# Kernel tuning notes

Hardware: AMD Instinct MI355X
Metric: run time of the kernel (lower is better)

The kernel has to match this reference:

```python
import jax, jax.numpy as jnp
import numpy as np

B, C, H, W = 4, 256, 64, 64
SCALE, K, COMP, G = 2, 5, 4, 1
MID = max(C // COMP, 16)                 # 64
ENC_OUT = K * K * SCALE * SCALE * G      # 100


def setup_inputs() -> dict:
    key = jax.random.key(0)
    k1, k2, k3 = jax.random.split(key, 3)
    x = jax.random.normal(k1, (B, C, H, W), jnp.float32)
    # comp: 1x1 conv C -> MID (store as matrix), enc: 3x3 conv MID -> ENC_OUT
    W_comp = jax.random.normal(k2, (MID, C), jnp.float32) * (1.0 / np.sqrt(C))
    b_comp = jnp.zeros((MID,), jnp.float32)
    W_enc = jax.random.normal(k3, (ENC_OUT, MID, 3, 3), jnp.float32) * (1.0 / np.sqrt(MID * 9))
    b_enc = jnp.zeros((ENC_OUT,), jnp.float32)
    return {"x": x, "W_comp": W_comp, "b_comp": b_comp, "W_enc": W_enc, "b_enc": b_enc}


def _unfold(x, k):
    """torch F.unfold with padding=(k-1)//2 -> (b, c, k*k, h, w), kh-major then kw."""
    b, c, h, w = x.shape
    p = (k - 1) // 2
    xp = jnp.pad(x, ((0, 0), (0, 0), (p, p), (p, p)))
    patches = jnp.stack(
        [xp[:, :, i:i + h, j:j + w] for i in range(k) for j in range(k)], axis=2
    )
    return patches  # (b, c, k*k, h, w)


def _carafe(x, W_comp, b_comp, W_enc, b_enc):
    b, c, h, w = x.shape
    s, k, g = SCALE, K, G
    # 1x1 compress conv + inplace relu
    feat = jax.nn.relu(jnp.einsum('bchw,mc->bmhw', x, W_comp) + b_comp[None, :, None, None])
    # 3x3 kernel-encoder conv, padding=1 (SAME)
    wk = jax.lax.conv_general_dilated(
        feat, W_enc, window_strides=(1, 1), padding='SAME',
        dimension_numbers=('NCHW', 'OIHW', 'NCHW')
    ) + b_enc[None, :, None, None]
    wk = wk.reshape(b, g, s * s, k * k, h, w)
    wk = jax.nn.softmax(wk, axis=3)  # softmax over k*k taps
    # unfold input and do the content-aware weighted gather-sum without the
    # (b,g,c/g,s*s,k*k,h,w) blow-up: contract over the k*k tap axis directly.
    xu = _unfold(x, k).reshape(b, g, c // g, k * k, h, w)
    out = jnp.einsum('bgpkhw,bgckhw->bgcphw', wk, xu)  # (b,g,c/g,s*s,h,w)
    # pixel rearrangement exactly as in the torch code:
    # view(b,c,s*s,h,w) -> permute(0,1,3,4,2) -> view(b,c,h*s,w*s)
    out = out.reshape(b, c, s * s, h, w)
    out = jnp.transpose(out, (0, 1, 3, 4, 2))
    out = out.reshape(b, c, h * s, w * s)
    return out


def reference(x, W_comp, b_comp, W_enc, b_enc):
    return _carafe(x, W_comp, b_comp, W_enc, b_enc)
```

## Files before the change

kernel.cpp:

```cpp
#include <hip/hip_runtime.h>

#define OFF_FEAT 0
#define OFF_WET  1048576
#define OFF_WCT  1122304
#define OFF_WK   1138688
#define WS_FLOATS 2777088

__global__ __launch_bounds__(256) void prep_kernel(
    const float* __restrict__ Wc, const float* __restrict__ We,
    float* __restrict__ ws) {
    int i = blockIdx.x * 256 + threadIdx.x;
    if (i < 16384) {
        int c = i >> 6, m = i & 63;
        ws[OFF_WCT + i] = Wc[m * 256 + c];
    }
    if (i < 73728) {
        int mrs = i >> 7, rem = i & 127;
        int p = rem >> 5, kk = rem & 31;
        ws[OFF_WET + i] = (kk < 25) ? We[(p * 25 + kk) * 576 + mrs] : 0.f;
    }
}

__global__ __launch_bounds__(256) void compress_kernel(
    const float* __restrict__ x, const float* __restrict__ bc,
    const float* __restrict__ ws, float* __restrict__ feat) {
    int blk = blockIdx.x;
    int pxg = blk >> 1, mh = blk & 1;
    int pixbase = pxg << 8;
    int b = pixbase >> 12, pl = pixbase & 4095;
    int t = threadIdx.x;
    const float* wct = ws + OFF_WCT + mh * 32;
    const float* xp = x + (((long long)b * 256) << 12) + pl + t;
    float acc[32];
#pragma unroll
    for (int q = 0; q < 32; q++) acc[q] = 0.f;
#pragma unroll 4
    for (int c = 0; c < 256; c++) {
        float xv = xp[(size_t)c << 12];
        const float* wr = wct + (c << 6);
#pragma unroll
        for (int q = 0; q < 32; q++) acc[q] += xv * wr[q];
    }
    int m0 = mh << 5;
#pragma unroll
    for (int q = 0; q < 32; q++) {
        float v = acc[q] + bc[m0 + q];
        feat[((b * 64 + m0 + q) << 12) + pl + t] = v > 0.f ? v : 0.f;
    }
}

__global__ __launch_bounds__(512, 4) void enc_kernel(
    const float* __restrict__ be, const float* __restrict__ ws,
    float* __restrict__ wkout) {
    __shared__ float fs[4224];
    int t = threadIdx.x;
    int blk = blockIdx.x;
    int tile = blk >> 1, ph2 = blk & 1;
    int b = tile >> 6, t6 = tile & 63;
    int i0 = (t6 >> 3) << 3, j0 = (t6 & 7) << 3;
    int pix = t & 63;
    int li = pix >> 3, lj = pix & 7;
    int g = __builtin_amdgcn_readfirstlane(t >> 6);
    int pp = g >> 2;
    int p = (ph2 << 1) | pp;
    int k0 = (g & 3) << 3;
    const float* feat = ws + OFF_FEAT;
    const float* wet = ws + OFF_WET + p * 32 + k0;

    float acc[8];
#pragma unroll
    for (int q = 0; q < 8; q++) acc[q] = 0.f;

    for (int phase = 0; phase < 2; phase++) {
        int mb = phase << 5;
        for (int idx = t; idx < 3200; idx += 512) {
            int m = idx / 100, pos = idx - m * 100;
            int r = pos / 10, s = pos - r * 10;
            int gi = i0 + r - 1, gj = j0 + s - 1;
            float v = 0.f;
            if ((unsigned)gi < 64u && (unsigned)gj < 64u)
                v = feat[(b * 64 + mb + m) * 4096 + (gi << 6) + gj];
            fs[m * 120 + r * 12 + s] = v;
        }
        __syncthreads();

#pragma unroll 2
        for (int m = 0; m < 32; m++) {
            const float* fb = fs + m * 120 + li * 12 + lj;
            float f9[9];
#pragma unroll
            for (int r = 0; r < 3; r++)
#pragma unroll
                for (int s = 0; s < 3; s++) f9[r * 3 + s] = fb[r * 12 + s];
            const float* wrow = wet + (mb + m) * 1152;
#pragma unroll
            for (int rs = 0; rs < 9; rs++) {
                float f = f9[rs];
                const float* wr = wrow + rs * 128;
#pragma unroll
                for (int q = 0; q < 8; q++) acc[q] += f * wr[q];
            }
        }
        __syncthreads();
    }

#pragma unroll
    for (int q = 0; q < 8; q++) {
        int k = k0 + q;
        if (k < 25) fs[pix * 66 + pp * 33 + k] = acc[q] + be[p * 25 + k];
    }
    __syncthreads();

    if (t < 128) {
        int sp = t >> 6, spx = t & 63;
        const float* lg = fs + spx * 66 + sp * 33;
        float sv[25], mx = -1e30f;
#pragma unroll
        for (int k = 0; k < 25; k++) { sv[k] = lg[k]; mx = fmaxf(mx, sv[k]); }
        float s = 0.f;
#pragma unroll
        for (int k = 0; k < 25; k++) { sv[k] = __expf(sv[k] - mx); s += sv[k]; }
        float inv = 1.f / s;
        int preal = (ph2 << 1) | sp;
        int pgl = ((i0 + (spx >> 3)) << 6) + j0 + (spx & 7);
        float* wp = wkout + (preal * 25) * 16384 + (b << 12) + pgl;
#pragma unroll
        for (int k = 0; k < 25; k++) wp[k * 16384] = sv[k] * inv;
    }
}

__global__ __launch_bounds__(256) void gather_kernel(
    const float* __restrict__ x, const float* __restrict__ ws,
    float* __restrict__ out) {
    __shared__ float xs[16 * 5 * 68];
    int t = threadIdx.x;
    int blk = blockIdx.x;
    int cc = blk & 15;
    int bi = blk >> 4;
    int b = bi >> 6, i = bi & 63;
    int j = t & 63;
    int g = t >> 6;
    int ph = g >> 1, ch = g & 1;

    float w0[25], w1[25];
    {
        const float* wp = ws + OFF_WK + (ph * 50) * 16384 + (b << 12) + (i << 6) + j;
#pragma unroll
        for (int k = 0; k < 25; k++) {
            w0[k] = wp[k * 16384];
            w1[k] = wp[(25 + k) * 16384];
        }
    }

    {
        int lane = t & 63, cd0 = t >> 6;
        for (int cd = cd0; cd < 80; cd += 4) {
            int c = cd / 5, dy = cd - c * 5;
            int gi = i - 2 + dy;
            float v = 0.f;
            if ((unsigned)gi < 64u)
                v = x[((b * 256 + (cc << 4) + c) << 12) + (gi << 6) + lane];
            float* row = xs + cd * 68;
            row[2 + lane] = v;
            if (lane < 2) row[lane] = 0.f;
            if (lane >= 62) row[lane + 4] = 0.f;
        }
    }
    __syncthreads();

    for (int c2 = ch; c2 < 16; c2 += 2) {
        const float* xb = xs + (c2 * 5) * 68 + j;
        float a0 = 0.f, a1 = 0.f;
#pragma unroll
        for (int dy = 0; dy < 5; dy++) {
#pragma unroll
            for (int dx = 0; dx < 5; dx++) {
                float xv = xb[dy * 68 + dx];
                int k = dy * 5 + dx;
                a0 += xv * w0[k];
                a1 += xv * w1[k];
            }
        }
        int c = (cc << 4) + c2;
        float2 o2 = make_float2(a0, a1);
        *(float2*)(out + (((b * 256 + c) << 12) + (i << 6) + j) * 4 + ph * 2) = o2;
    }
}

__global__ __launch_bounds__(512) void carafe_fused(
    const float* __restrict__ x, const float* __restrict__ Wc,
    const float* __restrict__ bc, const float* __restrict__ We,
    const float* __restrict__ be, float* __restrict__ out) {
    __shared__ float xs[32 * 144];
    __shared__ float fw[6656];
    __shared__ float wst[3600];
    const int t = threadIdx.x;
    const int blk = blockIdx.x;
    const int b = blk >> 6, tile = blk & 63;
    const int i0 = (tile >> 3) << 3, j0 = (tile & 7) << 3;
    const int wid = t >> 6, pix = t & 63;
    const int li = pix >> 3, lj = pix & 7;
    float facc[13];
#pragma unroll
    for (int q = 0; q < 13; q++) facc[q] = 0.f;
    for (int cc = 0; cc < 8; cc++) {
        for (int idx = t; idx < 32 * 144; idx += 512) {
            int c = idx / 144, pos = idx - c * 144;
            int r = pos / 12, u = pos - r * 12;
            int gi = i0 + r - 2, gj = j0 + u - 2;
            float v = 0.f;
            if ((unsigned)gi < 64u && (unsigned)gj < 64u)
                v = x[(((b * 256 + cc * 32 + c) << 12) + (gi << 6) + gj)];
            xs[idx] = v;
        }
        __syncthreads();
#pragma unroll
        for (int q = 0; q < 13; q++) {
            int idx = q * 512 + t;
            if (idx < 6400) {
                int m = idx / 100, pos = idx - m * 100;
                int fi = pos / 10, fj = pos - fi * 10;
                int tp = (fi + 1) * 12 + fj + 1;
                const float* wr = Wc + m * 256 + cc * 32;
                float a = facc[q];
                for (int c = 0; c < 32; c++) a += xs[c * 144 + tp] * wr[c];
                facc[q] = a;
            }
        }
        __syncthreads();
    }
#pragma unroll
    for (int q = 0; q < 13; q++) {
        int idx = q * 512 + t;
        if (idx < 6400) {
            int m = idx / 100, pos = idx - m * 100;
            int fi = pos / 10, fj = pos - fi * 10;
            int gi = i0 + fi - 1, gj = j0 + fj - 1;
            float v = facc[q] + bc[m];
            v = v > 0.f ? v : 0.f;
            if ((unsigned)gi >= 64u || (unsigned)gj >= 64u) v = 0.f;
            fw[idx] = v;
        }
    }
    float acc[13];
#pragma unroll
    for (int q = 0; q < 13; q++) acc[q] = 0.f;
    for (int mb = 0; mb < 16; mb++) {
        for (int idx = t; idx < 3600; idx += 512) {
            int mm = idx / 900, rem = idx - mm * 900;
            int o = rem / 9, rs = rem - o * 9;
            wst[idx] = We[o * 576 + (mb * 4 + mm) * 9 + rs];
        }
        __syncthreads();
#pragma unroll
        for (int mm = 0; mm < 4; mm++) {
            const float* fb = fw + (mb * 4 + mm) * 100 + li * 10 + lj;
            float f9[9];
#pragma unroll
            for (int r = 0; r < 3; r++)
#pragma unroll
                for (int s = 0; s < 3; s++) f9[r * 3 + s] = fb[r * 10 + s];
#pragma unroll
            for (int q = 0; q < 13; q++) {
                int o = q * 8 + wid;
                if (o < 100) {
                    const float* wr = wst + mm * 900 + o * 9;
                    float a = acc[q];
#pragma unroll
                    for (int rs = 0; rs < 9; rs++) a += f9[rs] * wr[rs];
                    acc[q] = a;
                }
            }
        }
        __syncthreads();
    }
#pragma unroll
    for (int q = 0; q < 13; q++) {
        int o = q * 8 + wid;
        if (o < 100) fw[pix * 104 + o] = acc[q];
    }
    __syncthreads();
    float sv[25];
    float inv = 0.f;
    const int sp = t >> 6, spx = t & 63;
    const bool act = (t < 256);
    if (act) {
        float mx = -1e30f;
#pragma unroll
        for (int k = 0; k < 25; k++) {
            sv[k] = fw[spx * 104 + sp * 25 + k] + be[sp * 25 + k];
            mx = fmaxf(mx, sv[k]);
        }
        float s = 0.f;
#pragma unroll
        for (int k = 0; k < 25; k++) { sv[k] = __expf(sv[k] - mx); s += sv[k]; }
        inv = 1.f / s;
    }
    __syncthreads();
    if (act) {
#pragma unroll
        for (int k = 0; k < 25; k++) fw[spx * 104 + k * 4 + sp] = sv[k] * inv;
    }
    __syncthreads();
    float w[25][4];
    const float4* wp = (const float4*)(fw + pix * 104);
#pragma unroll
    for (int k = 0; k < 25; k++) {
        float4 ww = wp[k];
        w[k][0] = ww.x; w[k][1] = ww.y; w[k][2] = ww.z; w[k][3] = ww.w;
    }
    const int pgl = ((i0 + li) << 6) + (j0 + lj);
    for (int cc = 0; cc < 8; cc++) {
        for (int idx = t; idx < 32 * 144; idx += 512) {
            int c = idx / 144, pos = idx - c * 144;
            int r = pos / 12, u = pos - r * 12;
            int gi = i0 + r - 2, gj = j0 + u - 2;
            float v = 0.f;
            if ((unsigned)gi < 64u && (unsigned)gj < 64u)
                v = x[(((b * 256 + cc * 32 + c) << 12) + (gi << 6) + gj)];
            xs[idx] = v;
        }
        __syncthreads();
        for (int c8 = wid; c8 < 32; c8 += 8) {
            const float* xc = xs + c8 * 144 + li * 12 + lj;
            float a0 = 0.f, a1 = 0.f, a2 = 0.f, a3 = 0.f;
#pragma unroll
            for (int dy = 0; dy < 5; dy++) {
#pragma unroll
                for (int dx = 0; dx < 5; dx++) {
                    float xv = xc[dy * 12 + dx];
                    const int k = dy * 5 + dx;
                    a0 += xv * w[k][0];
                    a1 += xv * w[k][1];
                    a2 += xv * w[k][2];
                    a3 += xv * w[k][3];
                }
            }
            int c = cc * 32 + c8;
            float4 o4 = make_float4(a0, a1, a2, a3);
            *(float4*)(out + (((long long)(b * 256 + c)) << 14) + pgl * 4) = o4;
        }
        __syncthreads();
    }
}

extern "C" void kernel_launch(void* const* d_in, const int* in_sizes, int n_in,
                              void* d_out, int out_size, void* d_ws, size_t ws_size,
                              hipStream_t stream) {
    const float* x  = (const float*)d_in[0];
    const float* Wc = (const float*)d_in[1];
    const float* bc = (const float*)d_in[2];
    const float* We = (const float*)d_in[3];
    const float* be = (const float*)d_in[4];
    float* out = (float*)d_out;

    if (ws_size >= (size_t)WS_FLOATS * sizeof(float)) {
        float* ws = (float*)d_ws;
        prep_kernel<<<288, 256, 0, stream>>>(Wc, We, ws);
        compress_kernel<<<128, 256, 0, stream>>>(x, bc, ws, ws + OFF_FEAT);
        enc_kernel<<<512, 512, 0, stream>>>(be, ws, ws + OFF_WK);
        gather_kernel<<<4096, 256, 0, stream>>>(x, ws, out);
    } else {
        carafe_fused<<<256, 512, 0, stream>>>(x, Wc, bc, We, be, out);
    }
}
```

Measured before the change: 220.8 us.

## Restructure compress kernel with lane-per-channel mapping and pixel-major feat layout

The compress 1x1 conv now maps each lane to one of the 64 output channels and each wavefront to four pixels. The pixel values are read as a wave-uniform float4, and the launch grows from 128 to 1024 blocks so far more work is in flight. The intermediate feature map is stored pixel-major (channel innermost), so compress writes are coalesced, and the encoder's shared-memory staging reads that new layout. The shared tile row stride is padded to 121 to avoid bank conflicts. The trade-off is that the encoder's global gather loads are now strided by 64 floats across spatial positions.

Measured after the change: 194.3 us. -12.0%, faster.

```diff
diff --git a/kernel.cpp b/kernel.cpp
--- a/kernel.cpp
+++ b/kernel.cpp
@@ -24,29 +24,29 @@
 __global__ __launch_bounds__(256) void compress_kernel(
     const float* __restrict__ x, const float* __restrict__ bc,
     const float* __restrict__ ws, float* __restrict__ feat) {
-    int blk = blockIdx.x;
-    int pxg = blk >> 1, mh = blk & 1;
-    int pixbase = pxg << 8;
-    int b = pixbase >> 12, pl = pixbase & 4095;
     int t = threadIdx.x;
-    const float* wct = ws + OFF_WCT + mh * 32;
-    const float* xp = x + (((long long)b * 256) << 12) + pl + t;
-    float acc[32];
-#pragma unroll
-    for (int q = 0; q < 32; q++) acc[q] = 0.f;
+    int lane = t & 63;
+    int px0 = __builtin_amdgcn_readfirstlane((blockIdx.x << 4) + ((t >> 6) << 2));
+    int b = px0 >> 12, pl = px0 & 4095;
+    const float* wct = ws + OFF_WCT;
+    const float* xw = x + (((size_t)(b * 256)) << 12) + pl;
+    float acc0 = 0.f, acc1 = 0.f, acc2 = 0.f, acc3 = 0.f;
 #pragma unroll 4
     for (int c = 0; c < 256; c++) {
-        float xv = xp[(size_t)c << 12];
-        const float* wr = wct + (c << 6);
-#pragma unroll
-        for (int q = 0; q < 32; q++) acc[q] += xv * wr[q];
-    }
-    int m0 = mh << 5;
-#pragma unroll
-    for (int q = 0; q < 32; q++) {
-        float v = acc[q] + bc[m0 + q];
-        feat[((b * 64 + m0 + q) << 12) + pl + t] = v > 0.f ? v : 0.f;
-    }
+        float w = wct[(c << 6) + lane];
+        const float4 xv = *(const float4*)(xw + ((size_t)c << 12));
+        acc0 += xv.x * w;
+        acc1 += xv.y * w;
+        acc2 += xv.z * w;
+        acc3 += xv.w * w;
+    }
+    float bv = bc[lane];
+    float v0 = acc0 + bv, v1 = acc1 + bv, v2 = acc2 + bv, v3 = acc3 + bv;
+    float* fp = feat + (((size_t)((b << 12) + pl)) << 6) + lane;
+    fp[0]       = v0 > 0.f ? v0 : 0.f;
+    fp[64]      = v1 > 0.f ? v1 : 0.f;
+    fp[128]     = v2 > 0.f ? v2 : 0.f;
+    fp[192]     = v3 > 0.f ? v3 : 0.f;
 }
 
 __global__ __launch_bounds__(512, 4) void enc_kernel(
@@ -74,19 +74,19 @@
     for (int phase = 0; phase < 2; phase++) {
         int mb = phase << 5;
         for (int idx = t; idx < 3200; idx += 512) {
-            int m = idx / 100, pos = idx - m * 100;
+            int m = idx & 31, pos = idx >> 5;
             int r = pos / 10, s = pos - r * 10;
             int gi = i0 + r - 1, gj = j0 + s - 1;
             float v = 0.f;
             if ((unsigned)gi < 64u && (unsigned)gj < 64u)
-                v = feat[(b * 64 + mb + m) * 4096 + (gi << 6) + gj];
-            fs[m * 120 + r * 12 + s] = v;
+                v = feat[(((size_t)((b << 12) + (gi << 6) + gj)) << 6) + mb + m];
+            fs[m * 121 + r * 12 + s] = v;
         }
         __syncthreads();
 
 #pragma unroll 2
         for (int m = 0; m < 32; m++) {
-            const float* fb = fs + m * 120 + li * 12 + lj;
+            const float* fb = fs + m * 121 + li * 12 + lj;
             float f9[9];
 #pragma unroll
             for (int r = 0; r < 3; r++)
@@ -357,7 +357,7 @@
     if (ws_size >= (size_t)WS_FLOATS * sizeof(float)) {
         float* ws = (float*)d_ws;
         prep_kernel<<<288, 256, 0, stream>>>(Wc, We, ws);
-        compress_kernel<<<128, 256, 0, stream>>>(x, bc, ws, ws + OFF_FEAT);
+        compress_kernel<<<1024, 256, 0, stream>>>(x, bc, ws, ws + OFF_FEAT);
         enc_kernel<<<512, 512, 0, stream>>>(be, ws, ws + OFF_WK);
         gather_kernel<<<4096, 256, 0, stream>>>(x, ws, out);
     } else {
```
